# Optimization experiments

Measured on AMD Instinct MI355X. Metric: run time of the kernel, lower is better.

The kernel has to match this reference:

```python
import jax, jax.numpy as jnp
import numpy as np

N, E, T = 20000, 200000, 400000
HID, DOWN, CO, DR = 128, 32, 64, 16


def _normalize(v):
    # F.normalize(dim=-1): v / max(||v||_2, eps)
    n = jnp.linalg.norm(v, axis=-1, keepdims=True)
    return v / jnp.maximum(n, 1e-12)


def setup_inputs() -> dict:
    key = jax.random.key(0)
    ks = jax.random.split(key, 16)
    return {
        "x": jax.random.normal(ks[0], (N, HID), jnp.float32),
        "robs": jax.random.normal(ks[1], (E, DR), jnp.float32),
        "shbs": jax.random.normal(ks[2], (T, DR), jnp.float32),
        "coeffs": jax.random.normal(ks[3], (N, DR, CO), jnp.float32),
        "edge_index": jax.random.randint(ks[4], (2, E), 0, N),
        "idx_j": jax.random.randint(ks[5], (T,), 0, N),
        "idx_k": jax.random.randint(ks[6], (T,), 0, N),
        "edge_idx_kj": jax.random.randint(ks[7], (T,), 0, E),
        "edge_idx_ji": jax.random.randint(ks[8], (T,), 0, E),
        # Dense params stored as [in, out]; y = x @ W (+ b)
        "W_node1": jax.random.normal(ks[9], (HID, HID), jnp.float32) / np.sqrt(HID).astype(np.float32),
        "b_node1": jnp.zeros((HID,), jnp.float32),
        "W_node2": jax.random.normal(ks[10], (HID, DOWN), jnp.float32) / np.sqrt(HID).astype(np.float32),
        "b_node2": jnp.zeros((DOWN,), jnp.float32),
        "W_co1": jax.random.normal(ks[11], (CO, HID), jnp.float32) / np.sqrt(CO).astype(np.float32),
        "W_co2": jax.random.normal(ks[12], (HID, DOWN), jnp.float32) / np.sqrt(HID).astype(np.float32),
        "W_up": jax.random.normal(ks[13], (DOWN, HID), jnp.float32) / np.sqrt(DOWN).astype(np.float32),
    }


def reference(x, robs, shbs, coeffs, edge_index, idx_j, idx_k, edge_idx_kj,
              edge_idx_ji, W_node1, b_node1, W_node2, b_node2, W_co1, W_co2, W_up):
    silu = jax.nn.silu
    edge_src, edge_dst = edge_index[0], edge_index[1]

    # node_lin: act -> Dense(hid,hid,bias) -> act -> Dense(hid,down,bias)
    x_d = silu(silu(x) @ W_node1 + b_node1) @ W_node2 + b_node2      # [N, DOWN]

    # coeffs_lin: act -> Dense(co,hid) -> act -> Dense(hid,down), no bias
    c = silu(silu(coeffs) @ W_co1) @ W_co2                           # [N, DR, DOWN]

    # triplet interaction
    c_k = c[idx_k]                                                   # [T, DR, DOWN]
    coeffs_kj = _normalize(c_k * c[idx_j] + c_k)                     # [T, DR, DOWN]
    tw = (shbs * robs[edge_idx_kj])[..., None] * coeffs_kj           # [T, DR, DOWN]
    tw = jax.ops.segment_sum(tw, edge_idx_ji, num_segments=robs.shape[0])  # [E, DR, DOWN]

    # edge interaction
    c_d = c[edge_dst]
    coeffs_ji = _normalize((c_d * c[edge_src] + c_d) * tw)           # [E, DR, DOWN]
    r = _normalize(jnp.einsum('ed,edh->eh', robs, coeffs_ji))        # [E, DOWN]

    # aggregate to nodes and up-project
    agg = jax.ops.segment_sum(x_d[edge_dst] * r, edge_src, num_segments=x.shape[0])  # [N, DOWN]
    return agg @ W_up                                                # [N, HID]
```

## Files before the change

### kernel.cpp

```cpp
#include <hip/hip_runtime.h>
#include <hip/hip_bf16.h>

#define N_NODES 20000
#define N_EDGES 200000
#define N_TRIP  400000
#define HID 128
#define DOWN 32
#define CO 64
#define DR 16

#define NODE_BLOCKS 1250
#define CO_BLOCKS   5000
#define TRIP_BLOCKS 1563
#define SLOTS 6

typedef __attribute__((ext_vector_type(8))) _Float16 half8;
typedef __attribute__((ext_vector_type(2))) _Float16 half2v;
typedef __attribute__((ext_vector_type(4))) float f32x4;
typedef __attribute__((ext_vector_type(2))) float f32x2;

__device__ __forceinline__ float silu_f(float v) {
    return v / (1.0f + __expf(-v));
}

template <int CTRL>
__device__ __forceinline__ float dpp_add(float x) {
    int a = __builtin_amdgcn_update_dpp(0, __float_as_int(x), CTRL, 0xF, 0xF, true);
    return x + __int_as_float(a);
}
__device__ __forceinline__ float quad_sum(float x) {
    return dpp_add<0x4E>(dpp_add<0xB1>(x));
}

__device__ __forceinline__ half2v h2of(const half8 v, int i) {
    half2v r; r[0] = v[2 * i]; r[1] = v[2 * i + 1]; return r;
}

__device__ __forceinline__ void trip_unit(const half8 hk, const half8 hj,
                                          float sw, bool valid, f32x2* tw2) {
    half2v u2[4];
    float ss = 0.0f;
    #pragma unroll
    for (int i = 0; i < 4; ++i) {
        half2v a = h2of(hk, i), b = h2of(hj, i);
        u2[i] = a * b + a;
        ss = __builtin_amdgcn_fdot2(u2[i], u2[i], ss, false);
    }
    ss = quad_sum(ss);
    float w = valid ? sw * __frsqrt_rn(fmaxf(ss, 1e-24f)) : 0.0f;
    #pragma unroll
    for (int i = 0; i < 4; ++i) {
        f32x2 uf = {(float)u2[i][0], (float)u2[i][1]};
        tw2[i] += uf * w;
    }
}

__global__ __launch_bounds__(256) void k_pre(
    const int* __restrict__ idxk, const int* __restrict__ idxj,
    const int* __restrict__ eji, const int* __restrict__ ekj,
    const float* __restrict__ shbs, const float* __restrict__ robs,
    const float* __restrict__ Wc1, const float* __restrict__ Wc2,
    int* __restrict__ head, int4* __restrict__ trip,
    _Float16* __restrict__ wprod, float* __restrict__ agg,
    _Float16* __restrict__ W1t, _Float16* __restrict__ W2t,
    int* __restrict__ cnt, int2* __restrict__ trip4) {
    const int tid = threadIdx.x;
    if (blockIdx.x < TRIP_BLOCKS) {
        int t = blockIdx.x * 256 + tid;
        if (t < N_TRIP) {
            int e = __builtin_nontemporal_load(&eji[t]);
            int slot = atomicAdd(&cnt[e], 1) - (int)0xAAAAAAAA;
            int nk = __builtin_nontemporal_load(&idxk[t]);
            int nj = __builtin_nontemporal_load(&idxj[t]);
            if (slot < SLOTS) {
                int2 r; r.x = nk | (nj << 15); r.y = t;
                trip4[(size_t)e * SLOTS + slot] = r;
            } else {
                int4 r; r.x = nk; r.y = nj;
                r.z = atomicExch(&head[e], t);
                r.w = 0;
                trip[t] = r;
            }
        }
        int z0 = blockIdx.x * 512 + tid;
        if (z0 < N_NODES * DOWN) agg[z0] = 0.0f;
        if (z0 + 256 < N_NODES * DOWN) agg[z0 + 256] = 0.0f;
    } else {
        int bb = blockIdx.x - TRIP_BLOCKS;
        int w0 = bb * 4096 + tid;
        #pragma unroll
        for (int k = 0; k < 16; ++k) {
            int w = w0 + k * 256;
            if (w < N_TRIP * DR) {
                int t = w >> 4, dr = w & 15;
                float sh = __builtin_nontemporal_load(&shbs[w]);
                wprod[w] = (_Float16)(sh * robs[ekj[t] * DR + dr]);
            }
        }
        int i2 = bb * 256 + tid;
        if (i2 < HID * CO)
            W1t[i2] = (_Float16)Wc1[(i2 & (CO - 1)) * HID + (i2 >> 6)];
        if (i2 < DOWN * HID)
            W2t[i2] = (_Float16)Wc2[(i2 & (HID - 1)) * DOWN + (i2 >> 7)];
    }
}

__global__ __launch_bounds__(256) void k_nodeco(
    const float* __restrict__ x, const float* __restrict__ W1,
    const float* __restrict__ b1, const float* __restrict__ W2,
    const float* __restrict__ b2, float* __restrict__ x_d,
    const float* __restrict__ cf, const _Float16* __restrict__ W1t,
    const _Float16* __restrict__ W2t, _Float16* __restrict__ ch) {
    __shared__ __align__(16) char smem[4 * 16 * 136 * 2];
    const int wave = threadIdx.x >> 6, lane = threadIdx.x & 63;

    if (blockIdx.x < NODE_BLOCKS) {
        float (*sx)[4][HID] = (float (*)[4][HID])smem;
        float (*sh)[4][HID] = (float (*)[4][HID])(smem + 8192);
        const int row0 = (blockIdx.x * 4 + wave) * 4;

        #pragma unroll
        for (int r = 0; r < 4; ++r) {
            sx[wave][r][lane]      = silu_f(__builtin_nontemporal_load(&x[(row0 + r) * HID + lane]));
            sx[wave][r][lane + 64] = silu_f(__builtin_nontemporal_load(&x[(row0 + r) * HID + lane + 64]));
        }
        __syncthreads();

        float acc[4][2] = {};
        for (int k = 0; k < HID; ++k) {
            float wa = W1[k * HID + lane];
            float wb = W1[k * HID + lane + 64];
            #pragma unroll
            for (int r = 0; r < 4; ++r) {
                float s = sx[wave][r][k];
                acc[r][0] = fmaf(s, wa, acc[r][0]);
                acc[r][1] = fmaf(s, wb, acc[r][1]);
            }
        }
        float ba = b1[lane], bb = b1[lane + 64];
        #pragma unroll
        for (int r = 0; r < 4; ++r) {
            sh[wave][r][lane]      = silu_f(acc[r][0] + ba);
            sh[wave][r][lane + 64] = silu_f(acc[r][1] + bb);
        }
        __syncthreads();

        const int m = lane & 31, kh = lane >> 5;
        float a2[4] = {};
        for (int kk = 0; kk < 64; ++kk) {
            int k = kh * 64 + kk;
            float w = W2[k * DOWN + m];
            #pragma unroll
            for (int r = 0; r < 4; ++r) a2[r] = fmaf(sh[wave][r][k], w, a2[r]);
        }
        #pragma unroll
        for (int r = 0; r < 4; ++r) a2[r] += __shfl_xor(a2[r], 32);
        if (kh == 0) {
            float bm = b2[m];
            #pragma unroll
            for (int r = 0; r < 4; ++r) x_d[(row0 + r) * DOWN + m] = a2[r] + bm;
        }
    } else {
        _Float16 (*sh)[16 * 136] = (_Float16 (*)[16 * 136])smem;
        const int m = lane & 15, q = lane >> 4;
        const int row0 = (blockIdx.x - NODE_BLOCKS) * 64 + wave * 16;

        const float* ar = cf + (row0 + m) * CO + q * 8;
        f32x4 a0 = __builtin_nontemporal_load((const f32x4*)ar);
        f32x4 a1 = __builtin_nontemporal_load(((const f32x4*)ar) + 1);
        f32x4 a2v = __builtin_nontemporal_load((const f32x4*)(ar + 32));
        f32x4 a3v = __builtin_nontemporal_load(((const f32x4*)(ar + 32)) + 1);
        half8 aA, aB;
        #pragma unroll
        for (int j = 0; j < 4; ++j) {
            aA[j]     = (_Float16)silu_f(a0[j]);
            aA[j + 4] = (_Float16)silu_f(a1[j]);
            aB[j]     = (_Float16)silu_f(a2v[j]);
            aB[j + 4] = (_Float16)silu_f(a3v[j]);
        }

        const half8* b1p = (const half8*)W1t;
        f32x4 acc[8];
        #pragma unroll
        for (int nt = 0; nt < 8; ++nt) {
            f32x4 z = {0.0f, 0.0f, 0.0f, 0.0f};
            half8 b0 = b1p[(nt * 16 + m) * 8 + q];
            half8 b1h = b1p[(nt * 16 + m) * 8 + 4 + q];
            z       = __builtin_amdgcn_mfma_f32_16x16x32_f16(aA, b0, z, 0, 0, 0);
            acc[nt] = __builtin_amdgcn_mfma_f32_16x16x32_f16(aB, b1h, z, 0, 0, 0);
        }

        _Float16* shw = sh[wave];
        #pragma unroll
        for (int nt = 0; nt < 8; ++nt) {
            #pragma unroll
            for (int r = 0; r < 4; ++r)
                shw[(q * 4 + r) * 136 + nt * 16 + m] = (_Float16)silu_f(acc[nt][r]);
        }

        const half8* b2p = (const half8*)W2t;
        f32x4 c0 = {0.0f, 0.0f, 0.0f, 0.0f}, c1 = {0.0f, 0.0f, 0.0f, 0.0f};
        #pragma unroll
        for (int ks = 0; ks < 4; ++ks) {
            half8 a = *(const half8*)(shw + m * 136 + ks * 32 + q * 8);
            half8 bb0 = b2p[m * 16 + ks * 4 + q];
            half8 bb1 = b2p[(16 + m) * 16 + ks * 4 + q];
            c0 = __builtin_amdgcn_mfma_f32_16x16x32_f16(a, bb0, c0, 0, 0, 0);
            c1 = __builtin_amdgcn_mfma_f32_16x16x32_f16(a, bb1, c1, 0, 0, 0);
        }
        #pragma unroll
        for (int r = 0; r < 4; ++r) {
            int rg = (row0 + q * 4 + r) * DOWN;
            ch[rg + m]      = (_Float16)c0[r];
            ch[rg + 16 + m] = (_Float16)c1[r];
        }
    }
}

__global__ __launch_bounds__(256) void k_edge(
    const _Float16* __restrict__ ch, const float* __restrict__ x_d,
    const float* __restrict__ robs, const int4* __restrict__ trip,
    const _Float16* __restrict__ wprod,
    const int* __restrict__ esrc, const int* __restrict__ edst,
    const int* __restrict__ head, float* __restrict__ agg,
    const int2* __restrict__ trip4, const int e0) {
    __shared__ float rbuf[4][DOWN];
    const int wave = threadIdx.x >> 6, lane = threadIdx.x & 63;
    const int e = __builtin_amdgcn_readfirstlane(e0 + blockIdx.x * 4 + wave);
    const int dr = lane >> 2, q = lane & 3;
    const half8* cp = (const half8*)ch;

    const int en_s = __builtin_nontemporal_load(&esrc[e]);
    const int en_d = __builtin_nontemporal_load(&edst[e]);
    half8 hd = cp[en_d * 64 + lane];
    half8 hs = cp[en_s * 64 + lane];
    float rob = __builtin_nontemporal_load(&robs[e * DR + dr]);
    float xd = (lane < DOWN) ? x_d[en_d * DOWN + lane] : 0.0f;

    const int2* t4 = trip4 + (size_t)e * SLOTS;
    const int4 sA = ((const int4*)t4)[0];
    const int4 sB = ((const int4*)t4)[1];
    const bool v0 = sA.y >= 0, v1 = sA.w >= 0;
    const bool v2 = sB.y >= 0, v3 = sB.w >= 0;
    const int k0 = v0 ? (sA.x & 32767) : 0;
    const int j0 = v0 ? (int)((unsigned)sA.x >> 15) : 0;
    const int z0 = v0 ? sA.y : 0;
    const int k1 = v1 ? (sA.z & 32767) : k0;
    const int j1 = v1 ? (int)((unsigned)sA.z >> 15) : j0;
    const int z1 = v1 ? sA.w : z0;
    const int k2 = v2 ? (sB.x & 32767) : k0;
    const int j2 = v2 ? (int)((unsigned)sB.x >> 15) : j0;
    const int z2 = v2 ? sB.y : z0;
    const int k3 = v3 ? (sB.z & 32767) : k0;
    const int j3 = v3 ? (int)((unsigned)sB.z >> 15) : j0;
    const int z3 = v3 ? sB.w : z0;

    half8 hk0 = cp[k0 * 64 + lane], hj0 = cp[j0 * 64 + lane];
    half8 hk1 = cp[k1 * 64 + lane], hj1 = cp[j1 * 64 + lane];
    half8 hk2 = cp[k2 * 64 + lane], hj2 = cp[j2 * 64 + lane];
    half8 hk3 = cp[k3 * 64 + lane], hj3 = cp[j3 * 64 + lane];
    float sw0 = (float)__builtin_nontemporal_load(&wprod[(size_t)z0 * DR + dr]);
    float sw1 = (float)__builtin_nontemporal_load(&wprod[(size_t)z1 * DR + dr]);
    float sw2 = (float)__builtin_nontemporal_load(&wprod[(size_t)z2 * DR + dr]);
    float sw3 = (float)__builtin_nontemporal_load(&wprod[(size_t)z3 * DR + dr]);

    f32x2 tw2[4];
    #pragma unroll
    for (int i = 0; i < 4; ++i) tw2[i] = (f32x2){0.0f, 0.0f};

    if (v0) {
        trip_unit(hk0, hj0, sw0, true, tw2);
        trip_unit(hk1, hj1, sw1, v1, tw2);
    }
    if (v2) {
        trip_unit(hk2, hj2, sw2, true, tw2);
        trip_unit(hk3, hj3, sw3, v3, tw2);
    }
    if (v3) {
        const int4 sC = ((const int4*)t4)[2];
        const bool v4 = sC.y >= 0, v5 = sC.w >= 0;
        if (v4) {
            const int k4 = sC.x & 32767;
            const int j4 = (int)((unsigned)sC.x >> 15);
            const int z4 = sC.y;
            const int k5 = v5 ? (sC.z & 32767) : k4;
            const int j5 = v5 ? (int)((unsigned)sC.z >> 15) : j4;
            const int z5 = v5 ? sC.w : z4;
            half8 hk4 = cp[k4 * 64 + lane], hj4 = cp[j4 * 64 + lane];
            half8 hk5 = cp[k5 * 64 + lane], hj5 = cp[j5 * 64 + lane];
            float sw4 = (float)__builtin_nontemporal_load(&wprod[(size_t)z4 * DR + dr]);
            float sw5 = (float)__builtin_nontemporal_load(&wprod[(size_t)z5 * DR + dr]);
            trip_unit(hk4, hj4, sw4, true, tw2);
            trip_unit(hk5, hj5, sw5, v5, tw2);
        }
        if (v5) {
            int t = __builtin_amdgcn_readfirstlane(head[e]);
            while (t >= 0) {
                const int4 tr = trip[t];
                half8 hk = cp[tr.x * 64 + lane];
                half8 hj = cp[tr.y * 64 + lane];
                const float sw = (float)__builtin_nontemporal_load(&wprod[(size_t)t * DR + dr]);
                trip_unit(hk, hj, sw, true, tw2);
                t = __builtin_amdgcn_readfirstlane(tr.z);
            }
        }
    }

    f32x2 v2e[4];
    float ss2 = 0.0f;
    #pragma unroll
    for (int i = 0; i < 4; ++i) {
        half2v d = h2of(hd, i), s = h2of(hs, i);
        half2v p = d * s + d;
        f32x2 pf = {(float)p[0], (float)p[1]};
        v2e[i] = pf * tw2[i];
        ss2 = fmaf(v2e[i][0], v2e[i][0], fmaf(v2e[i][1], v2e[i][1], ss2));
    }
    ss2 = quad_sum(ss2);
    float inv2 = __frsqrt_rn(fmaxf(ss2, 1e-24f));

    float rj[8];
    #pragma unroll
    for (int i = 0; i < 4; ++i) {
        rj[2 * i]     = v2e[i][0] * inv2 * rob;
        rj[2 * i + 1] = v2e[i][1] * inv2 * rob;
    }
    #pragma unroll
    for (int j = 0; j < 8; ++j) {
        rj[j] = dpp_add<0x124>(rj[j]);
        rj[j] = dpp_add<0x128>(rj[j]);
        rj[j] += __shfl_xor(rj[j], 16);
        rj[j] += __shfl_xor(rj[j], 32);
    }
    float s3 = 0.0f;
    #pragma unroll
    for (int j = 0; j < 8; ++j) s3 = fmaf(rj[j], rj[j], s3);
    s3 = quad_sum(s3);
    float inv3 = __frsqrt_rn(fmaxf(s3, 1e-24f));

    if (lane < 4) {
        #pragma unroll
        for (int j = 0; j < 8; ++j) rbuf[wave][q * 8 + j] = rj[j] * inv3;
    }
    if (lane < DOWN) {
        atomicAdd(&agg[en_s * DOWN + lane], xd * rbuf[wave][lane]);
    }
}

__global__ __launch_bounds__(256) void k_up(
    const float* __restrict__ agg, const float* __restrict__ Wup,
    float* __restrict__ out) {
    const int wave = threadIdx.x >> 6, lane = threadIdx.x & 63;
    const int row0 = (blockIdx.x * 4 + wave) * 4;
    float acc[4][2] = {};
    for (int k = 0; k < DOWN; ++k) {
        float wa = Wup[k * HID + lane];
        float wb = Wup[k * HID + lane + 64];
        #pragma unroll
        for (int r = 0; r < 4; ++r) {
            float a = __builtin_nontemporal_load(&agg[(row0 + r) * DOWN + k]);
            acc[r][0] = fmaf(a, wa, acc[r][0]);
            acc[r][1] = fmaf(a, wb, acc[r][1]);
        }
    }
    #pragma unroll
    for (int r = 0; r < 4; ++r) {
        out[(row0 + r) * HID + lane]      = acc[r][0];
        out[(row0 + r) * HID + lane + 64] = acc[r][1];
    }
}

extern "C" void kernel_launch(void* const* d_in, const int* in_sizes, int n_in,
                              void* d_out, int out_size, void* d_ws, size_t ws_size,
                              hipStream_t stream) {
    const float* x    = (const float*)d_in[0];
    const float* robs = (const float*)d_in[1];
    const float* shbs = (const float*)d_in[2];
    const float* cf   = (const float*)d_in[3];
    const int*   eidx = (const int*)d_in[4];
    const int*   idxj = (const int*)d_in[5];
    const int*   idxk = (const int*)d_in[6];
    const int*   ekj  = (const int*)d_in[7];
    const int*   eji  = (const int*)d_in[8];
    const float* W1   = (const float*)d_in[9];
    const float* b1   = (const float*)d_in[10];
    const float* W2   = (const float*)d_in[11];
    const float* b2   = (const float*)d_in[12];
    const float* Wc1  = (const float*)d_in[13];
    const float* Wc2  = (const float*)d_in[14];
    const float* Wup  = (const float*)d_in[15];
    const int* esrc = eidx;
    const int* edst = eidx + N_EDGES;
    float* out = (float*)d_out;

    float*    x_d   = (float*)d_ws;
    float*    agg   = x_d + (size_t)N_NODES * DOWN;
    int4*     trip  = (int4*)(agg + (size_t)N_NODES * DOWN);
    int*      head  = (int*)(trip + N_TRIP);
    _Float16* wprod = (_Float16*)(head + N_EDGES);
    _Float16* ch    = wprod + (size_t)N_TRIP * DR;
    _Float16* W1t   = ch + (size_t)N_NODES * DR * DOWN;
    _Float16* W2t   = W1t + HID * CO;
    int*      cnt   = (int*)(W2t + DOWN * HID);
    int2*     trip4 = (int2*)(cnt + N_EDGES);

    k_pre   <<<2 * TRIP_BLOCKS, 256, 0, stream>>>(idxk, idxj, eji, ekj, shbs,
                                                  robs, Wc1, Wc2, head, trip,
                                                  wprod, agg, W1t, W2t, cnt, trip4);
    k_nodeco<<<NODE_BLOCKS + CO_BLOCKS, 256, 0, stream>>>(x, W1, b1, W2, b2, x_d,
                                                          cf, W1t, W2t, ch);
    k_edge  <<<N_EDGES / 8, 256, 0, stream>>>(ch, x_d, robs, trip, wprod,
                                              esrc, edst, head, agg, trip4, 0);
    k_edge  <<<N_EDGES / 8, 256, 0, stream>>>(ch, x_d, robs, trip, wprod,
                                              esrc, edst, head, agg, trip4,
                                              N_EDGES / 2);
    k_up    <<<N_NODES / 16, 256, 0, stream>>>(agg, Wup, out);
}
```

Measured before the change: 441.1 us.

## Move node MLP to fp16 MFMA and split edge kernel into four launches

The node-MLP branch of the node/coefficient kernel now runs on fp16 MFMA instead of scalar fp32 FMAs. It processes 16 rows per wave, and the prep kernel writes transposed fp16 copies of W_node1 and W_node2. This is meant to cut the ALU cost of the node MLP and the number of node blocks, at the price of lower precision in x_d. The edge kernel is also launched four times over quarter ranges instead of twice over halves, which changes its grid partitioning.

After: 446.0 us. About the same (+1.1%).

```diff
diff --git a/kernel.cpp b/kernel.cpp
--- a/kernel.cpp
+++ b/kernel.cpp
@@ -9,7 +9,7 @@
 #define CO 64
 #define DR 16
 
-#define NODE_BLOCKS 1250
+#define NODE_BLOCKS 313
 #define CO_BLOCKS   5000
 #define TRIP_BLOCKS 1563
 #define SLOTS 6
@@ -60,9 +60,11 @@
     const int* __restrict__ eji, const int* __restrict__ ekj,
     const float* __restrict__ shbs, const float* __restrict__ robs,
     const float* __restrict__ Wc1, const float* __restrict__ Wc2,
+    const float* __restrict__ W1, const float* __restrict__ W2n,
     int* __restrict__ head, int4* __restrict__ trip,
     _Float16* __restrict__ wprod, float* __restrict__ agg,
     _Float16* __restrict__ W1t, _Float16* __restrict__ W2t,
+    _Float16* __restrict__ W1nt, _Float16* __restrict__ W2nt,
     int* __restrict__ cnt, int2* __restrict__ trip4) {
     const int tid = threadIdx.x;
     if (blockIdx.x < TRIP_BLOCKS) {
@@ -102,70 +104,73 @@
             W1t[i2] = (_Float16)Wc1[(i2 & (CO - 1)) * HID + (i2 >> 6)];
         if (i2 < DOWN * HID)
             W2t[i2] = (_Float16)Wc2[(i2 & (HID - 1)) * DOWN + (i2 >> 7)];
+        if (i2 < HID * HID)
+            W1nt[i2] = (_Float16)W1[(i2 & (HID - 1)) * HID + (i2 >> 7)];
+        if (i2 < DOWN * HID)
+            W2nt[i2] = (_Float16)W2n[(i2 & (HID - 1)) * DOWN + (i2 >> 7)];
     }
 }
 
 __global__ __launch_bounds__(256) void k_nodeco(
-    const float* __restrict__ x, const float* __restrict__ W1,
-    const float* __restrict__ b1, const float* __restrict__ W2,
+    const float* __restrict__ x, const _Float16* __restrict__ W1nt,
+    const float* __restrict__ b1, const _Float16* __restrict__ W2nt,
     const float* __restrict__ b2, float* __restrict__ x_d,
     const float* __restrict__ cf, const _Float16* __restrict__ W1t,
     const _Float16* __restrict__ W2t, _Float16* __restrict__ ch) {
-    __shared__ __align__(16) char smem[4 * 16 * 136 * 2];
+    __shared__ __align__(16) _Float16 sh[4][16 * 136];
     const int wave = threadIdx.x >> 6, lane = threadIdx.x & 63;
+    const int m = lane & 15, q = lane >> 4;
+    _Float16* shw = sh[wave];
 
     if (blockIdx.x < NODE_BLOCKS) {
-        float (*sx)[4][HID] = (float (*)[4][HID])smem;
-        float (*sh)[4][HID] = (float (*)[4][HID])(smem + 8192);
-        const int row0 = (blockIdx.x * 4 + wave) * 4;
-
+        const int row0 = (blockIdx.x * 4 + wave) * 16;
+        if (row0 >= N_NODES) return;
+
+        const float* xr = x + (size_t)(row0 + m) * HID + q * 8;
+        half8 ax[4];
+        #pragma unroll
+        for (int ks = 0; ks < 4; ++ks) {
+            f32x4 p0 = __builtin_nontemporal_load((const f32x4*)(xr + ks * 32));
+            f32x4 p1 = __builtin_nontemporal_load((const f32x4*)(xr + ks * 32 + 4));
+            #pragma unroll
+            for (int j = 0; j < 4; ++j) {
+                ax[ks][j]     = (_Float16)silu_f(p0[j]);
+                ax[ks][j + 4] = (_Float16)silu_f(p1[j]);
+            }
+        }
+        const half8* w1p = (const half8*)W1nt;
+        #pragma unroll
+        for (int nt = 0; nt < 8; ++nt) {
+            f32x4 accv = {0.0f, 0.0f, 0.0f, 0.0f};
+            #pragma unroll
+            for (int ks = 0; ks < 4; ++ks) {
+                half8 b = w1p[(nt * 16 + m) * 16 + ks * 4 + q];
+                accv = __builtin_amdgcn_mfma_f32_16x16x32_f16(ax[ks], b, accv, 0, 0, 0);
+            }
+            float bc = b1[nt * 16 + m];
+            #pragma unroll
+            for (int r = 0; r < 4; ++r)
+                shw[(q * 4 + r) * 136 + nt * 16 + m] = (_Float16)silu_f(accv[r] + bc);
+        }
+        const half8* w2p = (const half8*)W2nt;
+        f32x4 c0 = {0.0f, 0.0f, 0.0f, 0.0f}, c1 = {0.0f, 0.0f, 0.0f, 0.0f};
+        #pragma unroll
+        for (int ks = 0; ks < 4; ++ks) {
+            half8 a = *(const half8*)(shw + m * 136 + ks * 32 + q * 8);
+            c0 = __builtin_amdgcn_mfma_f32_16x16x32_f16(a, w2p[m * 16 + ks * 4 + q], c0, 0, 0, 0);
+            c1 = __builtin_amdgcn_mfma_f32_16x16x32_f16(a, w2p[(16 + m) * 16 + ks * 4 + q], c1, 0, 0, 0);
+        }
+        float bm0 = b2[m], bm1 = b2[16 + m];
         #pragma unroll
         for (int r = 0; r < 4; ++r) {
-            sx[wave][r][lane]      = silu_f(__builtin_nontemporal_load(&x[(row0 + r) * HID + lane]));
-            sx[wave][r][lane + 64] = silu_f(__builtin_nontemporal_load(&x[(row0 + r) * HID + lane + 64]));
-        }
-        __syncthreads();
-
-        float acc[4][2] = {};
-        for (int k = 0; k < HID; ++k) {
-            float wa = W1[k * HID + lane];
-            float wb = W1[k * HID + lane + 64];
-            #pragma unroll
-            for (int r = 0; r < 4; ++r) {
-                float s = sx[wave][r][k];
-                acc[r][0] = fmaf(s, wa, acc[r][0]);
-                acc[r][1] = fmaf(s, wb, acc[r][1]);
-            }
-        }
-        float ba = b1[lane], bb = b1[lane + 64];
-        #pragma unroll
-        for (int r = 0; r < 4; ++r) {
-            sh[wave][r][lane]      = silu_f(acc[r][0] + ba);
-            sh[wave][r][lane + 64] = silu_f(acc[r][1] + bb);
-        }
-        __syncthreads();
-
-        const int m = lane & 31, kh = lane >> 5;
-        float a2[4] = {};
-        for (int kk = 0; kk < 64; ++kk) {
-            int k = kh * 64 + kk;
-            float w = W2[k * DOWN + m];
-            #pragma unroll
-            for (int r = 0; r < 4; ++r) a2[r] = fmaf(sh[wave][r][k], w, a2[r]);
-        }
-        #pragma unroll
-        for (int r = 0; r < 4; ++r) a2[r] += __shfl_xor(a2[r], 32);
-        if (kh == 0) {
-            float bm = b2[m];
-            #pragma unroll
-            for (int r = 0; r < 4; ++r) x_d[(row0 + r) * DOWN + m] = a2[r] + bm;
+            int rg = (row0 + q * 4 + r) * DOWN;
+            x_d[rg + m]      = c0[r] + bm0;
+            x_d[rg + 16 + m] = c1[r] + bm1;
         }
     } else {
-        _Float16 (*sh)[16 * 136] = (_Float16 (*)[16 * 136])smem;
-        const int m = lane & 15, q = lane >> 4;
         const int row0 = (blockIdx.x - NODE_BLOCKS) * 64 + wave * 16;
 
-        const float* ar = cf + (row0 + m) * CO + q * 8;
+        const float* ar = cf + (size_t)(row0 + m) * CO + q * 8;
         f32x4 a0 = __builtin_nontemporal_load((const f32x4*)ar);
         f32x4 a1 = __builtin_nontemporal_load(((const f32x4*)ar) + 1);
         f32x4 a2v = __builtin_nontemporal_load((const f32x4*)(ar + 32));
@@ -190,7 +195,6 @@
             acc[nt] = __builtin_amdgcn_mfma_f32_16x16x32_f16(aB, b1h, z, 0, 0, 0);
         }
 
-        _Float16* shw = sh[wave];
         #pragma unroll
         for (int nt = 0; nt < 8; ++nt) {
             #pragma unroll
@@ -403,16 +407,26 @@
     _Float16* W2t   = W1t + HID * CO;
     int*      cnt   = (int*)(W2t + DOWN * HID);
     int2*     trip4 = (int2*)(cnt + N_EDGES);
+    _Float16* W1nt  = (_Float16*)(trip4 + (size_t)N_EDGES * SLOTS);
+    _Float16* W2nt  = W1nt + HID * HID;
 
     k_pre   <<<2 * TRIP_BLOCKS, 256, 0, stream>>>(idxk, idxj, eji, ekj, shbs,
-                                                  robs, Wc1, Wc2, head, trip,
-                                                  wprod, agg, W1t, W2t, cnt, trip4);
-    k_nodeco<<<NODE_BLOCKS + CO_BLOCKS, 256, 0, stream>>>(x, W1, b1, W2, b2, x_d,
-                                                          cf, W1t, W2t, ch);
-    k_edge  <<<N_EDGES / 8, 256, 0, stream>>>(ch, x_d, robs, trip, wprod,
-                                              esrc, edst, head, agg, trip4, 0);
-    k_edge  <<<N_EDGES / 8, 256, 0, stream>>>(ch, x_d, robs, trip, wprod,
-                                              esrc, edst, head, agg, trip4,
-                                              N_EDGES / 2);
+                                                  robs, Wc1, Wc2, W1, W2,
+                                                  head, trip, wprod, agg,
+                                                  W1t, W2t, W1nt, W2nt,
+                                                  cnt, trip4);
+    k_nodeco<<<NODE_BLOCKS + CO_BLOCKS, 256, 0, stream>>>(x, W1nt, b1, W2nt, b2,
+                                                          x_d, cf, W1t, W2t, ch);
+    k_edge  <<<N_EDGES / 16, 256, 0, stream>>>(ch, x_d, robs, trip, wprod,
+                                               esrc, edst, head, agg, trip4, 0);
+    k_edge  <<<N_EDGES / 16, 256, 0, stream>>>(ch, x_d, robs, trip, wprod,
+                                               esrc, edst, head, agg, trip4,
+                                               N_EDGES / 4);
+    k_edge  <<<N_EDGES / 16, 256, 0, stream>>>(ch, x_d, robs, trip, wprod,
+                                               esrc, edst, head, agg, trip4,
+                                               N_EDGES / 2);
+    k_edge  <<<N_EDGES / 16, 256, 0, stream>>>(ch, x_d, robs, trip, wprod,
+                                               esrc, edst, head, agg, trip4,
+                                               3 * (N_EDGES / 4));
     k_up    <<<N_NODES / 16, 256, 0, stream>>>(agg, Wup, out);
 }
```
